# Kernel tuning notes

Measured on AMD Instinct MI355X. Metric: run time of the kernel, lower is better.

## Reference

```python
import jax, jax.numpy as jnp
import numpy as np

B, N, D = 1, 2048, 2048
H, DH, DR, MP = 16, 128, 64, 4
LOCAL = H * DH // MP  # per-shard qkv width
ATTN_MASK_VALUE = -1e10
LN_EPS = 1e-5


def setup_inputs() -> dict:
    key = jax.random.key(0)
    ks = jax.random.split(key, 5)
    s = 0.02
    return {
        "x": jax.random.normal(ks[0], (B, N, D), jnp.float32),
        "ln_scale": jnp.ones((D,), jnp.float32),
        "ln_offset": jnp.zeros((D,), jnp.float32),
        "w_qkv": jax.random.normal(ks[1], (D, 3 * H * DH), jnp.float32) * s,
        "w_attn_out": jax.random.normal(ks[2], (H * DH, D), jnp.float32) * s,
        "w_ff_in": jax.random.normal(ks[3], (D, 4 * D), jnp.float32) * s,
        "b_ff_in": jnp.zeros((4 * D,), jnp.float32),
        "w_ff_out": jax.random.normal(ks[4], (4 * D, D), jnp.float32) * s,
        "b_ff_out": jnp.zeros((D,), jnp.float32),
    }


def _rotate_every_two(x):
    # (..., d) -> interleaved (-x2, x1) pairs, GPT-J style
    x1 = x[..., ::2]
    x2 = x[..., 1::2]
    return jnp.stack((-x2, x1), axis=-1).reshape(x.shape)


def _fixed_pos_embedding(n, dim):
    inv_freq = 1.0 / (10000.0 ** (np.arange(0, dim, 2, dtype=np.float32) / dim))
    ang = np.einsum("i,j->ij", np.arange(n, dtype=np.float32), inv_freq)  # [n, dim/2]
    return jnp.asarray(np.sin(ang), jnp.float32), jnp.asarray(np.cos(ang), jnp.float32)


def _apply_rotary(x, sin, cos):
    # x: [b, n, h, d_rot]; sin/cos: [n, d_rot/2] repeated pairwise -> [1, n, 1, d_rot]
    sin = jnp.repeat(sin, 2, axis=-1)[None, :, None, :]
    cos = jnp.repeat(cos, 2, axis=-1)[None, :, None, :]
    return x * cos + _rotate_every_two(x) * sin


def reference(x, ln_scale, ln_offset, w_qkv, w_attn_out, w_ff_in, b_ff_in, w_ff_out, b_ff_out):
    # ---- LayerNorm (shared input to parallel attn + FFN) ----
    mu = jnp.mean(x, axis=-1, keepdims=True)
    var = jnp.var(x, axis=-1, keepdims=True)
    h = (x - mu) * jax.lax.rsqrt(var + LN_EPS) * ln_scale + ln_offset

    # ---- Causal self-attention with partial rotary ----
    qkv = (h @ w_qkv).reshape(B, N, MP, 3 * LOCAL)  # mp-sharded layout
    q, v, k = jnp.split(qkv, [LOCAL, 2 * LOCAL], axis=-1)
    heads = lambda t: t.reshape(B, N, H, DH)  # shard_heads: [b,n,mp,local] -> [b,n,h,dh]
    q, v, k = heads(q), heads(v), heads(k)

    sin, cos = _fixed_pos_embedding(N, DR)
    q = jnp.concatenate([_apply_rotary(q[..., :DR], sin, cos), q[..., DR:]], axis=-1)
    k = jnp.concatenate([_apply_rotary(k[..., :DR], sin, cos), k[..., DR:]], axis=-1)

    attn_scale = np.float32(np.sqrt(DH))
    logits = jnp.einsum("bihd,bjhd->bhij", q, k) / attn_scale
    causal_mask = jnp.triu(jnp.ones((N, N), dtype=bool), 1)
    logits = jnp.where(causal_mask, ATTN_MASK_VALUE, logits)
    attn_w = jax.nn.softmax(logits, axis=-1)
    attn_vec = jnp.einsum("bhij,bjhd->bihd", attn_w, v).reshape(B, N, H * DH)
    attn_out = attn_vec @ w_attn_out

    # ---- FFN (parallel branch, same LN input) ----
    ff_out = jax.nn.gelu(h @ w_ff_in + b_ff_in) @ w_ff_out + b_ff_out

    return attn_out + ff_out
```

## Files before the change

kernel.cpp:

```cpp
#include <hip/hip_runtime.h>
#include <hip/hip_bf16.h>

using bf16_t = __hip_bfloat16;
typedef __attribute__((ext_vector_type(8))) __bf16 bfrag;
typedef __attribute__((ext_vector_type(4))) float f32x4;

#define MFMA16(a, b, c) __builtin_amdgcn_mfma_f32_16x16x32_bf16((a), (b), (c), 0, 0, 0)

__device__ __forceinline__ void gload_lds16(const void* g, void* l) {
  __builtin_amdgcn_global_load_lds((const __attribute__((address_space(1))) void*)g,
                                   (__attribute__((address_space(3))) void*)l, 16, 0, 0);
}

__device__ __forceinline__ float bf2f(unsigned u) { return __uint_as_float(u << 16); }

__global__ __launch_bounds__(256) void transpose_cvt(const float* __restrict__ in,
    bf16_t* __restrict__ out, int K, int N) {
  __shared__ float t[64][65];
  const int n0 = blockIdx.x * 64, k0 = blockIdx.y * 64;
  const int tx = threadIdx.x & 15, ty = threadIdx.x >> 4;
#pragma unroll
  for (int i = 0; i < 4; ++i) {
    float4 v = *(const float4*)&in[(size_t)(k0 + i * 16 + ty) * N + n0 + tx * 4];
    t[i * 16 + ty][tx * 4 + 0] = v.x; t[i * 16 + ty][tx * 4 + 1] = v.y;
    t[i * 16 + ty][tx * 4 + 2] = v.z; t[i * 16 + ty][tx * 4 + 3] = v.w;
  }
  __syncthreads();
#pragma unroll
  for (int i = 0; i < 4; ++i) {
    const int n = i * 16 + ty;
    bf16_t w[4];
#pragma unroll
    for (int j = 0; j < 4; ++j) w[j] = bf16_t(t[tx * 4 + j][n]);
    *(uint2*)&out[(size_t)(n0 + n) * K + k0 + tx * 4] = *(const uint2*)w;
  }
}

__global__ __launch_bounds__(256) void ln_kernel(const float* __restrict__ x,
    const float* __restrict__ sc, const float* __restrict__ of, bf16_t* __restrict__ h) {
  __shared__ float red[8];
  const int n = blockIdx.x, tid = threadIdx.x;
  const float* xr = x + (size_t)n * 2048;
  float4 a = ((const float4*)xr)[tid * 2];
  float4 b = ((const float4*)xr)[tid * 2 + 1];
  float s = a.x + a.y + a.z + a.w + b.x + b.y + b.z + b.w;
  float q = a.x * a.x + a.y * a.y + a.z * a.z + a.w * a.w +
            b.x * b.x + b.y * b.y + b.z * b.z + b.w * b.w;
#pragma unroll
  for (int m = 32; m; m >>= 1) { s += __shfl_xor(s, m); q += __shfl_xor(q, m); }
  if ((tid & 63) == 0) { red[(tid >> 6) * 2] = s; red[(tid >> 6) * 2 + 1] = q; }
  __syncthreads();
  s = red[0] + red[2] + red[4] + red[6];
  q = red[1] + red[3] + red[5] + red[7];
  const float mu = s * (1.f / 2048.f);
  const float inv = rsqrtf(q * (1.f / 2048.f) - mu * mu + 1e-5f);
  const int base = tid * 8;
  float v[8] = {a.x, a.y, a.z, a.w, b.x, b.y, b.z, b.w};
  bf16_t* hr = h + (size_t)n * 2048 + base;
#pragma unroll
  for (int j = 0; j < 8; ++j) hr[j] = bf16_t((v[j] - mu) * inv * sc[base + j] + of[base + j]);
}

template <int EPI>
__global__ __launch_bounds__(512, 2) void gemm8p(
    const bf16_t* __restrict__ A, int lda, const bf16_t* __restrict__ BT, int ldb,
    const float* __restrict__ bias, float* __restrict__ Cf, bf16_t* __restrict__ Cb,
    int M, int N, int K, size_t splitStride) {
  extern __shared__ __align__(16) char lds[];
  const int tid = threadIdx.x, wid = tid >> 6, lane = tid & 63;
  const int lc = lane & 15, lg = lane >> 4;
  const int bm = blockIdx.y * 256, bn = blockIdx.x * 256;
  const int wr = wid >> 2, wc = wid & 3;
  const int NT = K >> 6, niter = NT >> 1;
  const int srow = tid >> 3;
  const int scol = (((tid & 7) ^ ((tid >> 3) & 7)) << 3);
  const bf16_t* Abase = A + (size_t)blockIdx.z * K + (size_t)(bm + srow) * lda + scol;
  const bf16_t* Bbase = BT + (size_t)blockIdx.z * K + (size_t)(bn + srow) * ldb + scol;
  auto SA = [&](int T, int h) {
    char* dst = lds + (T & 1) * 32768 + h * 16384 + wid * 1024;
    const bf16_t* src = Abase + (size_t)(h * 128) * lda + T * 64;
    gload_lds16(src, dst); gload_lds16(src + (size_t)64 * lda, dst + 8192);
  };
  auto SB = [&](int T, int h) {
    char* dst = lds + 65536 + (T & 1) * 32768 + h * 16384 + wid * 1024;
    const bf16_t* src = Bbase + (size_t)(h * 128) * ldb + T * 64;
    gload_lds16(src, dst); gload_lds16(src + (size_t)64 * ldb, dst + 8192);
  };
#define FRA(d, row, kk) (*(const bfrag*)(lds + (d) * 32768 + wr * 16384 + (row) * 128 + \
    ((((kk) * 4 + lg) ^ ((row) & 7)) << 4)))
#define FRB(d, row, kk) (*(const bfrag*)(lds + 65536 + (d) * 32768 + (wc >> 1) * 16384 + \
    (row) * 128 + ((((kk) * 4 + lg) ^ ((row) & 7)) << 4)))
#define PHASE_SYNC() do { __builtin_amdgcn_s_barrier(); \
    asm volatile("s_waitcnt lgkmcnt(0)" ::: "memory"); \
    __builtin_amdgcn_sched_barrier(0); __builtin_amdgcn_s_setprio(1); } while (0)
#define PHASE_END() do { __builtin_amdgcn_s_setprio(0); __builtin_amdgcn_s_barrier(); } while (0)
#define PHASE_END_VM(lastf) do { __builtin_amdgcn_s_setprio(0); \
    if (lastf) asm volatile("s_waitcnt vmcnt(0)" ::: "memory"); \
    else       asm volatile("s_waitcnt vmcnt(4)" ::: "memory"); \
    __builtin_amdgcn_s_barrier(); } while (0)

  SB(0, 0); SB(0, 1); SA(0, 0); SA(0, 1); SB(1, 0); SB(1, 1);
  asm volatile("s_waitcnt vmcnt(4)" ::: "memory");
  __builtin_amdgcn_s_barrier();

  f32x4 acc[8][4] = {};
  const int brl = (wc & 1) * 64 + lc;

  for (int k = 0; k < niter; ++k) {
    const int T1 = 2 * k + 1, T2 = 2 * k + 2, T3 = 2 * k + 3;
    const bool last = (k == niter - 1);
    bfrag aq[4][2], b01[2][2], b23[2][2];
#pragma unroll 1
    for (int d = 0; d < 2; ++d) {
#pragma unroll
      for (int m = 0; m < 4; ++m)
#pragma unroll
        for (int kk = 0; kk < 2; ++kk) aq[m][kk] = FRA(d, m * 16 + lc, kk);
#pragma unroll
      for (int n = 0; n < 2; ++n)
#pragma unroll
        for (int kk = 0; kk < 2; ++kk) b01[n][kk] = FRB(d, brl + n * 16, kk);
      if (d == 0) SA(T1, 0); else if (!last) SA(T2, 0);
      PHASE_SYNC();
#pragma unroll
      for (int kk = 0; kk < 2; ++kk)
#pragma unroll
        for (int m = 0; m < 4; ++m) {
          acc[m][0] = MFMA16(aq[m][kk], b01[0][kk], acc[m][0]);
          acc[m][1] = MFMA16(aq[m][kk], b01[1][kk], acc[m][1]);
        }
      PHASE_END();
#pragma unroll
      for (int n = 0; n < 2; ++n)
#pragma unroll
        for (int kk = 0; kk < 2; ++kk) b23[n][kk] = FRB(d, brl + (n + 2) * 16, kk);
      if (d == 0) SA(T1, 1); else if (!last) SA(T2, 1);
      PHASE_SYNC();
#pragma unroll
      for (int kk = 0; kk < 2; ++kk)
#pragma unroll
        for (int m = 0; m < 4; ++m) {
          acc[m][2] = MFMA16(aq[m][kk], b23[0][kk], acc[m][2]);
          acc[m][3] = MFMA16(aq[m][kk], b23[1][kk], acc[m][3]);
        }
      PHASE_END();
#pragma unroll
      for (int m = 0; m < 4; ++m)
#pragma unroll
        for (int kk = 0; kk < 2; ++kk) aq[m][kk] = FRA(d, (m + 4) * 16 + lc, kk);
      if (!last) { if (d == 0) SB(T2, 0); else SB(T3, 0); }
      PHASE_SYNC();
#pragma unroll
      for (int kk = 0; kk < 2; ++kk)
#pragma unroll
        for (int m = 0; m < 4; ++m) {
          acc[4 + m][2] = MFMA16(aq[m][kk], b23[0][kk], acc[4 + m][2]);
          acc[4 + m][3] = MFMA16(aq[m][kk], b23[1][kk], acc[4 + m][3]);
        }
      PHASE_END();
      if (!last) { if (d == 0) SB(T2, 1); else SB(T3, 1); }
      PHASE_SYNC();
#pragma unroll
      for (int kk = 0; kk < 2; ++kk)
#pragma unroll
        for (int m = 0; m < 4; ++m) {
          acc[4 + m][0] = MFMA16(aq[m][kk], b01[0][kk], acc[4 + m][0]);
          acc[4 + m][1] = MFMA16(aq[m][kk], b01[1][kk], acc[4 + m][1]);
        }
      PHASE_END_VM(last);
    }
  }
#undef FRA
#undef FRB
#undef PHASE_SYNC
#undef PHASE_END
#undef PHASE_END_VM
  char* W = lds + wid * 16384;
  if (EPI & 8) {
    bf16_t* Wb = (bf16_t*)W;
    bf16_t* Cbz = Cb + (size_t)blockIdx.z * splitStride;
#pragma unroll
    for (int mc = 0; mc < 2; ++mc) {
#pragma unroll
      for (int m4 = 0; m4 < 4; ++m4) {
#pragma unroll
        for (int n = 0; n < 4; ++n) {
          const int col = bn + wc * 64 + n * 16 + lc;
          float bv = (EPI & 1) ? bias[col] : 0.f;
#pragma unroll
          for (int i = 0; i < 4; ++i) {
            float v = acc[mc * 4 + m4][n][i];
            if (EPI & 1) v += bv;
            if (EPI & 2) v = 0.5f * v * (1.f + tanhf(0.7978845608028654f * (v + 0.044715f * v * v * v)));
            Wb[(m4 * 16 + lg * 4 + i) * 72 + n * 16 + lc] = bf16_t(v);
          }
        }
      }
      asm volatile("s_waitcnt lgkmcnt(0)" ::: "memory");
      __builtin_amdgcn_sched_barrier(0);
#pragma unroll
      for (int p = 0; p < 8; ++p) {
        const int rl = p * 8 + (lane >> 3), j = lane & 7;
        uint4 v = *(const uint4*)&Wb[rl * 72 + j * 8];
        const int grow = bm + wr * 128 + mc * 64 + rl;
        const int gcol = bn + wc * 64 + j * 8;
        *(uint4*)&Cbz[(size_t)grow * N + gcol] = v;
      }
      asm volatile("s_waitcnt lgkmcnt(0)" ::: "memory");
      __builtin_amdgcn_sched_barrier(0);
    }
  } else {
    float* Wf = (float*)W;
    float* Cfz = Cf + (size_t)blockIdx.z * splitStride;
#pragma unroll
    for (int mc = 0; mc < 4; ++mc) {
#pragma unroll
      for (int m2 = 0; m2 < 2; ++m2) {
#pragma unroll
        for (int n = 0; n < 4; ++n) {
          const int col = bn + wc * 64 + n * 16 + lc;
          float bv = (EPI & 1) ? bias[col] : 0.f;
#pragma unroll
          for (int i = 0; i < 4; ++i) {
            float v = acc[mc * 2 + m2][n][i];
            if (EPI & 1) v += bv;
            if (EPI & 2) v = 0.5f * v * (1.f + tanhf(0.7978845608028654f * (v + 0.044715f * v * v * v)));
            Wf[(m2 * 16 + lg * 4 + i) * 72 + n * 16 + lc] = v;
          }
        }
      }
      asm volatile("s_waitcnt lgkmcnt(0)" ::: "memory");
      __builtin_amdgcn_sched_barrier(0);
#pragma unroll
      for (int p = 0; p < 8; ++p) {
        const int rl = p * 4 + (lane >> 4), j = lane & 15;
        float4 v = *(const float4*)&Wf[rl * 72 + j * 4];
        const int grow = bm + wr * 128 + mc * 32 + rl;
        const int gcol = bn + wc * 64 + j * 4;
        *(float4*)&Cfz[(size_t)grow * N + gcol] = v;
      }
      asm volatile("s_waitcnt lgkmcnt(0)" ::: "memory");
      __builtin_amdgcn_sched_barrier(0);
    }
  }
}

template <int NP, bool ADDIN, bool BIAS>
__global__ __launch_bounds__(256) void reduceP(const float* __restrict__ p0,
    const float* __restrict__ p1, const float* __restrict__ p2,
    const float* __restrict__ p3, const float* __restrict__ bias,
    float* __restrict__ out, int total, int colmask) {
  const int i = (blockIdx.x * 256 + threadIdx.x) * 4;
  if (i >= total) return;
  float4 v = *(const float4*)(p0 + i);
  float4 w = *(const float4*)(p1 + i);
  v.x += w.x; v.y += w.y; v.z += w.z; v.w += w.w;
  if (NP == 4) {
    float4 u = *(const float4*)(p2 + i);
    float4 z = *(const float4*)(p3 + i);
    v.x += u.x + z.x; v.y += u.y + z.y; v.z += u.z + z.z; v.w += u.w + z.w;
  }
  if (BIAS) {
    float4 b = *(const float4*)(bias + (i & colmask));
    v.x += b.x; v.y += b.y; v.z += b.z; v.w += b.w;
  }
  if (ADDIN) {
    float4 o = *(const float4*)(out + i);
    v.x += o.x; v.y += o.y; v.z += o.z; v.w += o.w;
  }
  *(float4*)(out + i) = v;
}

__global__ __launch_bounds__(256) void reduce4b(const bf16_t* __restrict__ p0,
    const bf16_t* __restrict__ p1, const bf16_t* __restrict__ p2,
    const bf16_t* __restrict__ p3, float* __restrict__ out, int total) {
  const int i = (blockIdx.x * 256 + threadIdx.x) * 8;
  if (i >= total) return;
  uint4 a0 = *(const uint4*)(p0 + i);
  uint4 a1 = *(const uint4*)(p1 + i);
  uint4 a2 = *(const uint4*)(p2 + i);
  uint4 a3 = *(const uint4*)(p3 + i);
  const unsigned* u0 = (const unsigned*)&a0;
  const unsigned* u1 = (const unsigned*)&a1;
  const unsigned* u2 = (const unsigned*)&a2;
  const unsigned* u3 = (const unsigned*)&a3;
  float r[8];
#pragma unroll
  for (int j = 0; j < 8; ++j) {
    const int w = j >> 1, sh = (j & 1) * 16;
    r[j] = bf2f((u0[w] >> sh) & 0xffffu) + bf2f((u1[w] >> sh) & 0xffffu) +
           bf2f((u2[w] >> sh) & 0xffffu) + bf2f((u3[w] >> sh) & 0xffffu);
  }
  *(float4*)(out + i) = make_float4(r[0], r[1], r[2], r[3]);
  *(float4*)(out + i + 4) = make_float4(r[4], r[5], r[6], r[7]);
}

__global__ __launch_bounds__(128) void rope_kernel(const bf16_t* __restrict__ qkv,
    bf16_t* __restrict__ qh, bf16_t* __restrict__ kh, bf16_t* __restrict__ vT) {
  const int n = blockIdx.x, hh = blockIdx.y;
  const int d = threadIdx.x;
  const int mp = hh >> 2, hi = hh & 3;
  const bf16_t* row = qkv + (size_t)n * 6144 + mp * 1536 + hi * 128;
  float q = __bfloat162float(row[d]);
  float k = __bfloat162float(row[1024 + d]);
  if (d < 64) {
    const float ang = (float)n * powf(10000.f, -(float)(d & ~1) / 64.f);
    const float sn = sinf(ang), cs = cosf(ang);
    const float qp = __shfl_xor(q, 1), kp = __shfl_xor(k, 1);
    if (d & 1) { q = q * cs + qp * sn; k = k * cs + kp * sn; }
    else       { q = q * cs - qp * sn; k = k * cs - kp * sn; }
  }
  qh[((size_t)hh * 2048 + n) * 128 + d] = bf16_t(q * 0.08838834764831845f);
  kh[((size_t)hh * 2048 + n) * 128 + d] = bf16_t(k);
  vT[((size_t)hh * 128 + d) * 2048 + n] = row[512 + d];
}

__global__ __launch_bounds__(256) void attn_kernel(const bf16_t* __restrict__ qh,
    const bf16_t* __restrict__ kh, const bf16_t* __restrict__ vT,
    bf16_t* __restrict__ Op, float2* __restrict__ ml) {
  __shared__ alignas(16) char Kbuf[2][16384];
  __shared__ alignas(16) char Vbuf[2][16384];
  __shared__ alignas(16) bf16_t Ps[4][16 * 72];
  const int p = blockIdx.x, h = blockIdx.y, z = blockIdx.z;
  const int tid = threadIdx.x, wid = tid >> 6, lane = tid & 63;
  const int lc = lane & 15, lg = lane >> 4;
  const int krow = wid * 4 + (lane >> 4);
  const int vrow = wid * 8 + (lane >> 3);

  auto stage = [&](int kv0, int d) {
#pragma unroll
    for (int i = 0; i < 4; ++i) {
      const int kr = i * 16 + krow;
      const int kch = (lane & 15) ^ (kr & 15);
      gload_lds16(kh + ((size_t)h * 2048 + kv0 + kr) * 128 + kch * 8,
                  Kbuf[d] + i * 4096 + wid * 1024);
      const int vr = i * 32 + vrow;
      const int vch = (lane & 7) ^ (vr & 7);
      gload_lds16(vT + ((size_t)h * 128 + vr) * 2048 + kv0 + vch * 8,
                  Vbuf[d] + i * 4096 + wid * 1024);
    }
  };
#define FRK(d, row, ch) (*(const bfrag*)(Kbuf[d] + (row) * 256 + (((ch) ^ ((row) & 15)) << 4)))
#define FRV(d, row, ch) (*(const bfrag*)(Vbuf[d] + (row) * 128 + (((ch) ^ ((row) & 7)) << 4)))

#pragma unroll 1
  for (int half = 0; half < 2; ++half) {
    const int qt = half ? (31 - p) : p;
    const int nkv = qt + 1;
    const int lo = (z * nkv) / 3, hi = ((z + 1) * nkv) / 3;
    const int nj = hi - lo;
    const int qr = qt * 64 + wid * 16;
    const bf16_t* Qb = qh + ((size_t)h * 2048 + qr) * 128;
    bfrag qf[4];
#pragma unroll
    for (int ks = 0; ks < 4; ++ks)
      qf[ks] = *(const bfrag*)&Qb[lc * 128 + ks * 32 + lg * 8];
    f32x4 O[8] = {};
    float mr[4] = {-1e30f, -1e30f, -1e30f, -1e30f};
    float lsum[4] = {0.f, 0.f, 0.f, 0.f};

    if (nj > 0) {
      stage(lo * 64, 0);
      asm volatile("s_waitcnt vmcnt(0)" ::: "memory");
      __builtin_amdgcn_s_barrier();
    }
#pragma unroll 1
    for (int j = 0; j < nj; ++j) {
      const int kt = lo + j, d = j & 1;
      const int kv0 = kt * 64;
      if (j + 1 < nj) stage(kv0 + 64, d ^ 1);
      f32x4 s[4];
#pragma unroll
      for (int c = 0; c < 4; ++c) {
        f32x4 a = {};
#pragma unroll
        for (int ks = 0; ks < 4; ++ks) {
          bfrag kf = FRK(d, c * 16 + lc, ks * 4 + lg);
          a = MFMA16(qf[ks], kf, a);
        }
        s[c] = a;
      }
      if (kt == qt) {
#pragma unroll
        for (int c = 0; c < 4; ++c)
#pragma unroll
          for (int i = 0; i < 4; ++i)
            if (kv0 + c * 16 + lc > qr + lg * 4 + i) s[c][i] = -1e10f;
      }
      float pm[4];
#pragma unroll
      for (int i = 0; i < 4; ++i)
        pm[i] = fmaxf(fmaxf(s[0][i], s[1][i]), fmaxf(s[2][i], s[3][i]));
#pragma unroll
      for (int m = 1; m < 16; m <<= 1)
#pragma unroll
        for (int i = 0; i < 4; ++i) pm[i] = fmaxf(pm[i], __shfl_xor(pm[i], m));
      float al[4], rs[4];
#pragma unroll
      for (int i = 0; i < 4; ++i) {
        const float mn = fmaxf(mr[i], pm[i]);
        al[i] = __expf(mr[i] - mn);
        mr[i] = mn;
        rs[i] = 0.f;
      }
#pragma unroll
      for (int c = 0; c < 4; ++c)
#pragma unroll
        for (int i = 0; i < 4; ++i) {
          const float pv = __expf(s[c][i] - mr[i]);
          s[c][i] = pv; rs[i] += pv;
        }
#pragma unroll
      for (int m = 1; m < 16; m <<= 1)
#pragma unroll
        for (int i = 0; i < 4; ++i) rs[i] += __shfl_xor(rs[i], m);
#pragma unroll
      for (int i = 0; i < 4; ++i) lsum[i] = lsum[i] * al[i] + rs[i];
#pragma unroll
      for (int n = 0; n < 8; ++n)
#pragma unroll
        for (int i = 0; i < 4; ++i) O[n][i] *= al[i];
#pragma unroll
      for (int c = 0; c < 4; ++c)
#pragma unroll
        for (int i = 0; i < 4; ++i)
          Ps[wid][(lg * 4 + i) * 72 + c * 16 + lc] = bf16_t(s[c][i]);
#pragma unroll
      for (int k2 = 0; k2 < 2; ++k2) {
        bfrag pf = *(const bfrag*)((const char*)&Ps[wid][0] + lc * 144 + k2 * 64 + lg * 16);
#pragma unroll
        for (int n = 0; n < 8; ++n) {
          bfrag vf = FRV(d, n * 16 + lc, k2 * 4 + lg);
          O[n] = MFMA16(pf, vf, O[n]);
        }
      }
      if (j + 1 < nj) asm volatile("s_waitcnt vmcnt(0)" ::: "memory");
      asm volatile("s_waitcnt lgkmcnt(0)" ::: "memory");
      __builtin_amdgcn_s_barrier();
    }
    const size_t rb = (size_t)(z * 16 + h) * 2048 + qr;
#pragma unroll
    for (int n = 0; n < 8; ++n)
#pragma unroll
      for (int i = 0; i < 4; ++i)
        Op[(rb + lg * 4 + i) * 128 + n * 16 + lc] = bf16_t(O[n][i]);
    if (lc == 0) {
#pragma unroll
      for (int i = 0; i < 4; ++i)
        ml[rb + lg * 4 + i] = make_float2(mr[i], lsum[i]);
    }
    __builtin_amdgcn_s_barrier();
  }
#undef FRK
#undef FRV
}

__global__ __launch_bounds__(256) void attn_combine(const bf16_t* __restrict__ Op,
    const float2* __restrict__ ml, bf16_t* __restrict__ av) {
  const int idx = blockIdx.x * 256 + threadIdx.x;
  const int t = idx & 15, hr = idx >> 4;
  const int ZS = 16 * 2048;
  const size_t ZO = (size_t)ZS * 128;
  const float2 m0 = ml[hr], m1 = ml[ZS + hr], m2 = ml[2 * ZS + hr];
  const float M = fmaxf(fmaxf(m0.x, m1.x), m2.x);
  const float w0 = __expf(m0.x - M), w1 = __expf(m1.x - M), w2 = __expf(m2.x - M);
  const float inv = 1.f / (w0 * m0.y + w1 * m1.y + w2 * m2.y);
  const bf16_t* p0 = Op + (size_t)hr * 128 + t * 8;
  uint4 a0 = *(const uint4*)p0;
  uint4 a1 = *(const uint4*)(p0 + ZO);
  uint4 a2 = *(const uint4*)(p0 + 2 * ZO);
  const unsigned* u0 = (const unsigned*)&a0;
  const unsigned* u1 = (const unsigned*)&a1;
  const unsigned* u2 = (const unsigned*)&a2;
  bf16_t ov[8];
#pragma unroll
  for (int j = 0; j < 8; ++j) {
    const int w = j >> 1, sh = (j & 1) * 16;
    ov[j] = bf16_t((w0 * bf2f((u0[w] >> sh) & 0xffffu) +
                    w1 * bf2f((u1[w] >> sh) & 0xffffu) +
                    w2 * bf2f((u2[w] >> sh) & 0xffffu)) * inv);
  }
  const int row = hr & 2047, hh = hr >> 11;
  *(uint4*)(av + (size_t)row * 2048 + hh * 128 + t * 8) = *(const uint4*)ov;
}

extern "C" void kernel_launch(void* const* d_in, const int* in_sizes, int n_in,
                              void* d_out, int out_size, void* d_ws, size_t ws_size,
                              hipStream_t stream) {
  const float* x        = (const float*)d_in[0];
  const float* ln_scale = (const float*)d_in[1];
  const float* ln_offset= (const float*)d_in[2];
  const float* w_qkv    = (const float*)d_in[3];
  const float* w_ao     = (const float*)d_in[4];
  const float* w_ff_in  = (const float*)d_in[5];
  const float* b_ff_in  = (const float*)d_in[6];
  const float* w_ff_out = (const float*)d_in[7];
  const float* b_ff_out = (const float*)d_in[8];
  float* out = (float*)d_out;

  char* ws = (char*)d_ws;
  bf16_t* wqkvT   = (bf16_t*)(ws);
  bf16_t* waoT    = (bf16_t*)(ws + 25165824);
  bf16_t* wffinT  = (bf16_t*)(ws + 33554432);
  bf16_t* wffoutT = (bf16_t*)(ws + 67108864);
  bf16_t* h       = (bf16_t*)(ws + 100663296);
  bf16_t* qhb     = (bf16_t*)(ws + 109051904);
  bf16_t* khb     = (bf16_t*)(ws + 117440512);
  bf16_t* vTb     = (bf16_t*)(ws + 125829120);
  bf16_t* avb     = (bf16_t*)(ws + 134217728);
  bf16_t* qkvb    = (bf16_t*)(ws + 142606336);
  bf16_t* ff1b    = qkvb;
  bf16_t* pab     = qkvb;
  float*  pf      = (float*)(ws);
  bf16_t* Opart   = (bf16_t*)(ws);
  float2* mlpart  = (float2*)(ws + 167772160);

  hipFuncSetAttribute((const void*)gemm8p<0>,  hipFuncAttributeMaxDynamicSharedMemorySize, 131072);
  hipFuncSetAttribute((const void*)gemm8p<8>,  hipFuncAttributeMaxDynamicSharedMemorySize, 131072);
  hipFuncSetAttribute((const void*)gemm8p<11>, hipFuncAttributeMaxDynamicSharedMemorySize, 131072);

  dim3 b256(256), b512(512);
  transpose_cvt<<<dim3(96, 32),  b256, 0, stream>>>(w_qkv,    wqkvT,   2048, 6144);
  transpose_cvt<<<dim3(32, 32),  b256, 0, stream>>>(w_ao,     waoT,    2048, 2048);
  transpose_cvt<<<dim3(128, 32), b256, 0, stream>>>(w_ff_in,  wffinT,  2048, 8192);
  transpose_cvt<<<dim3(32, 128), b256, 0, stream>>>(w_ff_out, wffoutT, 8192, 2048);
  ln_kernel<<<dim3(2048), b256, 0, stream>>>(x, ln_scale, ln_offset, h);

  gemm8p<8><<<dim3(24, 8, 1), b512, 131072, stream>>>(h, 2048, wqkvT, 2048,
      nullptr, nullptr, qkvb, 2048, 6144, 2048, 0);
  rope_kernel<<<dim3(2048, 16), dim3(128), 0, stream>>>(qkvb, qhb, khb, vTb);

  attn_kernel<<<dim3(16, 16, 3), b256, 0, stream>>>(qhb, khb, vTb, Opart, mlpart);
  attn_combine<<<dim3(2048), b256, 0, stream>>>(Opart, mlpart, avb);

  gemm8p<8><<<dim3(8, 8, 4), b512, 131072, stream>>>(avb, 2048, waoT, 2048,
      nullptr, nullptr, pab, 2048, 2048, 512, (size_t)2048 * 2048);
  reduce4b<<<dim3(2048), b256, 0, stream>>>(pab, pab + 4194304, pab + 2 * 4194304,
      pab + 3 * 4194304, out, 4194304);

  gemm8p<11><<<dim3(32, 8, 1), b512, 131072, stream>>>(h, 2048, wffinT, 2048,
      b_ff_in, nullptr, ff1b, 2048, 8192, 2048, 0);

  gemm8p<0><<<dim3(8, 8, 4), b512, 131072, stream>>>(ff1b, 8192, wffoutT, 8192,
      nullptr, pf, nullptr, 2048, 2048, 2048, (size_t)2048 * 2048);
  reduceP<4, true, true><<<dim3(4096), b256, 0, stream>>>(pf, pf + 4194304,
      pf + 2 * 4194304, pf + 3 * 4194304, b_ff_out, out, 4194304, 2047);
}
```

Baseline: 416.6 us.

## Restructure GEMM main loop to prefetch next tile's fragments across phases

```diff
diff --git a/kernel.cpp b/kernel.cpp
--- a/kernel.cpp
+++ b/kernel.cpp
@@ -71,7 +71,7 @@
   const int lc = lane & 15, lg = lane >> 4;
   const int bm = blockIdx.y * 256, bn = blockIdx.x * 256;
   const int wr = wid >> 2, wc = wid & 3;
-  const int NT = K >> 6, niter = NT >> 1;
+  const int NT = K >> 6;
   const int srow = tid >> 3;
   const int scol = (((tid & 7) ^ ((tid >> 3) & 7)) << 3);
   const bf16_t* Abase = A + (size_t)blockIdx.z * K + (size_t)(bm + srow) * lda + scol;
@@ -86,95 +86,106 @@
     const bf16_t* src = Bbase + (size_t)(h * 128) * ldb + T * 64;
     gload_lds16(src, dst); gload_lds16(src + (size_t)64 * ldb, dst + 8192);
   };
-#define FRA(d, row, kk) (*(const bfrag*)(lds + (d) * 32768 + wr * 16384 + (row) * 128 + \
+#define FRA(D, row, kk) (*(const bfrag*)(lds + (D) * 32768 + wr * 16384 + (row) * 128 + \
     ((((kk) * 4 + lg) ^ ((row) & 7)) << 4)))
-#define FRB(d, row, kk) (*(const bfrag*)(lds + 65536 + (d) * 32768 + (wc >> 1) * 16384 + \
+#define FRB(D, row, kk) (*(const bfrag*)(lds + 65536 + (D) * 32768 + (wc >> 1) * 16384 + \
     (row) * 128 + ((((kk) * 4 + lg) ^ ((row) & 7)) << 4)))
-#define PHASE_SYNC() do { __builtin_amdgcn_s_barrier(); \
-    asm volatile("s_waitcnt lgkmcnt(0)" ::: "memory"); \
-    __builtin_amdgcn_sched_barrier(0); __builtin_amdgcn_s_setprio(1); } while (0)
-#define PHASE_END() do { __builtin_amdgcn_s_setprio(0); __builtin_amdgcn_s_barrier(); } while (0)
-#define PHASE_END_VM(lastf) do { __builtin_amdgcn_s_setprio(0); \
-    if (lastf) asm volatile("s_waitcnt vmcnt(0)" ::: "memory"); \
-    else       asm volatile("s_waitcnt vmcnt(4)" ::: "memory"); \
-    __builtin_amdgcn_s_barrier(); } while (0)
-
-  SB(0, 0); SB(0, 1); SA(0, 0); SA(0, 1); SB(1, 0); SB(1, 1);
-  asm volatile("s_waitcnt vmcnt(4)" ::: "memory");
+
+  SA(0, 0); SA(0, 1); SB(0, 0); SB(0, 1);
+  SA(1, 0); SA(1, 1); SB(1, 0); SB(1, 1);
+  asm volatile("s_waitcnt vmcnt(8)" ::: "memory");
   __builtin_amdgcn_s_barrier();
 
   f32x4 acc[8][4] = {};
+  bfrag aL[4][2], aH[4][2], b01A[2][2], b01B[2][2], b23v[2][2];
   const int brl = (wc & 1) * 64 + lc;
-
-  for (int k = 0; k < niter; ++k) {
-    const int T1 = 2 * k + 1, T2 = 2 * k + 2, T3 = 2 * k + 3;
-    const bool last = (k == niter - 1);
-    bfrag aq[4][2], b01[2][2], b23[2][2];
-#pragma unroll 1
-    for (int d = 0; d < 2; ++d) {
+#pragma unroll
+  for (int m = 0; m < 4; ++m)
+#pragma unroll
+    for (int kk = 0; kk < 2; ++kk) aL[m][kk] = FRA(0, m * 16 + lc, kk);
+#pragma unroll
+  for (int n = 0; n < 2; ++n)
+#pragma unroll
+    for (int kk = 0; kk < 2; ++kk) b01A[n][kk] = FRB(0, brl + n * 16, kk);
+
+  auto tile_body = [&](int T, int D, bfrag (&B01C)[2][2], bfrag (&B01N)[2][2]) {
+#pragma unroll
+    for (int n = 0; n < 2; ++n)
+#pragma unroll
+      for (int kk = 0; kk < 2; ++kk) b23v[n][kk] = FRB(D, brl + (n + 2) * 16, kk);
+    __builtin_amdgcn_s_barrier();
+    asm volatile("s_waitcnt lgkmcnt(4)" ::: "memory");
+    __builtin_amdgcn_s_setprio(1);
+#pragma unroll
+    for (int kk = 0; kk < 2; ++kk)
+#pragma unroll
+      for (int m = 0; m < 4; ++m) {
+        acc[m][0] = MFMA16(aL[m][kk], B01C[0][kk], acc[m][0]);
+        acc[m][1] = MFMA16(aL[m][kk], B01C[1][kk], acc[m][1]);
+      }
+    __builtin_amdgcn_s_setprio(0);
+#pragma unroll
+    for (int m = 0; m < 4; ++m)
+#pragma unroll
+      for (int kk = 0; kk < 2; ++kk) aH[m][kk] = FRA(D, (m + 4) * 16 + lc, kk);
+    __builtin_amdgcn_s_barrier();
+    asm volatile("s_waitcnt lgkmcnt(8)" ::: "memory");
+    __builtin_amdgcn_s_setprio(1);
+#pragma unroll
+    for (int kk = 0; kk < 2; ++kk)
+#pragma unroll
+      for (int m = 0; m < 4; ++m) {
+        acc[m][2] = MFMA16(aL[m][kk], b23v[0][kk], acc[m][2]);
+        acc[m][3] = MFMA16(aL[m][kk], b23v[1][kk], acc[m][3]);
+      }
+    __builtin_amdgcn_s_setprio(0);
+    if (T + 2 < NT) {
+      SA(T + 2, 0); SA(T + 2, 1);
+      asm volatile("s_waitcnt vmcnt(4)" ::: "memory");
+    } else {
+      asm volatile("s_waitcnt vmcnt(0)" ::: "memory");
+    }
+    __builtin_amdgcn_s_barrier();
+    asm volatile("s_waitcnt lgkmcnt(0)" ::: "memory");
+    __builtin_amdgcn_s_setprio(1);
+#pragma unroll
+    for (int kk = 0; kk < 2; ++kk)
+#pragma unroll
+      for (int m = 0; m < 4; ++m) {
+        acc[4 + m][2] = MFMA16(aH[m][kk], b23v[0][kk], acc[4 + m][2]);
+        acc[4 + m][3] = MFMA16(aH[m][kk], b23v[1][kk], acc[4 + m][3]);
+      }
+    __builtin_amdgcn_s_setprio(0);
+    if (T + 1 < NT) {
+#pragma unroll
+      for (int n = 0; n < 2; ++n)
+#pragma unroll
+        for (int kk = 0; kk < 2; ++kk) B01N[n][kk] = FRB((D) ^ 1, brl + n * 16, kk);
 #pragma unroll
       for (int m = 0; m < 4; ++m)
 #pragma unroll
-        for (int kk = 0; kk < 2; ++kk) aq[m][kk] = FRA(d, m * 16 + lc, kk);
-#pragma unroll
-      for (int n = 0; n < 2; ++n)
-#pragma unroll
-        for (int kk = 0; kk < 2; ++kk) b01[n][kk] = FRB(d, brl + n * 16, kk);
-      if (d == 0) SA(T1, 0); else if (!last) SA(T2, 0);
-      PHASE_SYNC();
-#pragma unroll
-      for (int kk = 0; kk < 2; ++kk)
-#pragma unroll
-        for (int m = 0; m < 4; ++m) {
-          acc[m][0] = MFMA16(aq[m][kk], b01[0][kk], acc[m][0]);
-          acc[m][1] = MFMA16(aq[m][kk], b01[1][kk], acc[m][1]);
-        }
-      PHASE_END();
-#pragma unroll
-      for (int n = 0; n < 2; ++n)
-#pragma unroll
-        for (int kk = 0; kk < 2; ++kk) b23[n][kk] = FRB(d, brl + (n + 2) * 16, kk);
-      if (d == 0) SA(T1, 1); else if (!last) SA(T2, 1);
-      PHASE_SYNC();
-#pragma unroll
-      for (int kk = 0; kk < 2; ++kk)
-#pragma unroll
-        for (int m = 0; m < 4; ++m) {
-          acc[m][2] = MFMA16(aq[m][kk], b23[0][kk], acc[m][2]);
-          acc[m][3] = MFMA16(aq[m][kk], b23[1][kk], acc[m][3]);
-        }
-      PHASE_END();
-#pragma unroll
-      for (int m = 0; m < 4; ++m)
-#pragma unroll
-        for (int kk = 0; kk < 2; ++kk) aq[m][kk] = FRA(d, (m + 4) * 16 + lc, kk);
-      if (!last) { if (d == 0) SB(T2, 0); else SB(T3, 0); }
-      PHASE_SYNC();
-#pragma unroll
-      for (int kk = 0; kk < 2; ++kk)
-#pragma unroll
-        for (int m = 0; m < 4; ++m) {
-          acc[4 + m][2] = MFMA16(aq[m][kk], b23[0][kk], acc[4 + m][2]);
-          acc[4 + m][3] = MFMA16(aq[m][kk], b23[1][kk], acc[4 + m][3]);
-        }
-      PHASE_END();
-      if (!last) { if (d == 0) SB(T2, 1); else SB(T3, 1); }
-      PHASE_SYNC();
-#pragma unroll
-      for (int kk = 0; kk < 2; ++kk)
-#pragma unroll
-        for (int m = 0; m < 4; ++m) {
-          acc[4 + m][0] = MFMA16(aq[m][kk], b01[0][kk], acc[4 + m][0]);
-          acc[4 + m][1] = MFMA16(aq[m][kk], b01[1][kk], acc[4 + m][1]);
-        }
-      PHASE_END_VM(last);
-    }
+        for (int kk = 0; kk < 2; ++kk) aL[m][kk] = FRA((D) ^ 1, m * 16 + lc, kk);
+    }
+    if (T + 2 < NT) { SB(T + 2, 0); SB(T + 2, 1); }
+    __builtin_amdgcn_s_barrier();
+    if (T + 1 < NT) asm volatile("s_waitcnt lgkmcnt(12)" ::: "memory");
+    __builtin_amdgcn_s_setprio(1);
+#pragma unroll
+    for (int kk = 0; kk < 2; ++kk)
+#pragma unroll
+      for (int m = 0; m < 4; ++m) {
+        acc[4 + m][0] = MFMA16(aH[m][kk], B01C[0][kk], acc[4 + m][0]);
+        acc[4 + m][1] = MFMA16(aH[m][kk], B01C[1][kk], acc[4 + m][1]);
+      }
+    __builtin_amdgcn_s_setprio(0);
+  };
+
+  for (int k = 0; k < (NT >> 1); ++k) {
+    tile_body(2 * k,     0, b01A, b01B);
+    tile_body(2 * k + 1, 1, b01B, b01A);
   }
 #undef FRA
 #undef FRB
-#undef PHASE_SYNC
-#undef PHASE_END
-#undef PHASE_END_VM
   char* W = lds + wid * 16384;
   if (EPI & 8) {
     bf16_t* Wb = (bf16_t*)W;
```

New measurement: 918.7 us. 121% more time.
